# Performance work log

Measured on AMD Instinct MI355X. Metric: run time of the kernel, lower is better.

The kernel has to match this reference:

```python
import jax, jax.numpy as jnp
import numpy as np

N = 100000        # num_nodes
F_IN = 512        # node_features
F_OUT = 2         # GCNConv out channels (hardcoded in module)
E = 3200000       # num edges (avg degree 32)


def setup_inputs() -> dict:
    key = jax.random.key(0)
    k = jax.random.split(key, 8)
    x = jax.random.normal(k[0], (N, F_IN), dtype=jnp.float32)
    edge_list = jax.random.randint(k[1], (2, E), 0, N, dtype=jnp.int64)
    edge_attr = jax.random.uniform(k[2], (E,), dtype=jnp.float32)
    # GCNConv params (glorot-ish scale)
    W = jax.random.normal(k[3], (F_IN, F_OUT), dtype=jnp.float32) / np.sqrt(F_IN)
    b = jnp.zeros((F_OUT,), dtype=jnp.float32)
    # fc head: Linear(num_nodes*2, 1)
    fc_w = jax.random.normal(k[4], (N * F_OUT,), dtype=jnp.float32) / np.sqrt(N * F_OUT)
    fc_b = jnp.zeros((), dtype=jnp.float32)
    return {"x": x, "edge_list": edge_list, "edge_attr": edge_attr,
            "W": W, "b": b, "fc_w": fc_w, "fc_b": fc_b}


def reference(x, edge_list, edge_attr, W, b, fc_w, fc_b):
    n = x.shape[0]
    row, col = edge_list[0], edge_list[1]
    # --- gcn_norm with add_self_loops=True (fill weight 1.0) ---
    loop = jnp.arange(n, dtype=edge_list.dtype)
    row_f = jnp.concatenate([row, loop])
    col_f = jnp.concatenate([col, loop])
    w_f = jnp.concatenate([edge_attr, jnp.ones((n,), dtype=edge_attr.dtype)])
    deg = jax.ops.segment_sum(w_f, col_f, num_segments=n)          # [N]
    deg_inv_sqrt = jnp.where(deg > 0, jax.lax.rsqrt(jnp.maximum(deg, 1e-30)), 0.0)
    norm = deg_inv_sqrt[row_f] * w_f * deg_inv_sqrt[col_f]          # [E+N]
    # --- linear transform then propagate (source row -> target col) ---
    h = x @ W                                                       # [N, 2]
    msg = h[row_f] * norm[:, None]                                  # [E+N, 2]
    out = jax.ops.segment_sum(msg, col_f, num_segments=n) + b      # [N, 2]
    # --- head: relu, (no dropout/noise: training=False), flatten, fc, sigmoid ---
    out = jax.nn.relu(out).reshape(-1)                              # [2N]
    logit = jnp.dot(out, fc_w) + fc_b
    return jax.nn.sigmoid(logit)
```

## Files before the change

### kernel.cpp

```cpp
#include <hip/hip_runtime.h>
#include <math.h>

#define N_NODES 100000
#define F_IN    512
#define E_EDGES 3200000

#define NR   16
#define RN   6250
#define REP  32
#define CHUNK (E_EDGES / REP)


__global__ __launch_bounds__(1024) void k_deg_tiled(const int* __restrict__ col,
                                                    const float* __restrict__ w,
                                                    float* __restrict__ rep_deg) {
    __shared__ float sdeg[RN];
    int r = blockIdx.x / REP, p = blockIdx.x % REP;
    int r0 = r * RN;
    for (int j = threadIdx.x; j < RN; j += 1024) sdeg[j] = 0.0f;
    __syncthreads();
    const int*   colc = col + p * CHUNK;
    const float* wc   = w   + p * CHUNK;
    for (int e4 = threadIdx.x * 4; e4 < CHUNK; e4 += 4096) {
        int4 c4 = *(const int4*)(colc + e4);
#pragma unroll
        for (int q = 0; q < 4; ++q) {
            unsigned j = (unsigned)((&c4.x)[q] - r0);
            if (j < RN) atomicAdd(&sdeg[j], wc[e4 + q]);
        }
    }
    __syncthreads();
    float* out = rep_deg + (size_t)blockIdx.x * RN;
    for (int j = threadIdx.x; j < RN; j += 1024) out[j] = sdeg[j];
}

__global__ void k_dis(const float* __restrict__ rep_deg,
                      float* __restrict__ dis, float* __restrict__ logit) {
    int i = blockIdx.x * blockDim.x + threadIdx.x;
    if (i < N_NODES) {
        int r = i / RN, j = i - r * RN;
        const float* base = rep_deg + (size_t)(r * REP) * RN + j;
        float d = 1.0f;
#pragma unroll
        for (int p = 0; p < REP; ++p) d += base[p * RN];
        dis[i] = rsqrtf(d);
    }
    if (i == 0) logit[0] = 0.0f;
}

__global__ __launch_bounds__(256) void k_gemv(const float* __restrict__ x,
                                              const float* __restrict__ W,
                                              const float* __restrict__ dis,
                                              float* __restrict__ g) {
    int row  = (blockIdx.x * blockDim.x + threadIdx.x) >> 6;
    int lane = threadIdx.x & 63;
    if (row >= N_NODES) return;
    const float* xr = x + (size_t)row * F_IN;
    float a0 = 0.0f, a1 = 0.0f;
#pragma unroll
    for (int c = 0; c < 2; ++c) {
        int k = c * 256 + lane * 4;
        float4 xv  = *(const float4*)(xr + k);
        float4 w01 = *(const float4*)(W + 2 * k);
        float4 w23 = *(const float4*)(W + 2 * k + 4);
        a0 += xv.x * w01.x + xv.y * w01.z + xv.z * w23.x + xv.w * w23.z;
        a1 += xv.x * w01.y + xv.y * w01.w + xv.z * w23.y + xv.w * w23.w;
    }
#pragma unroll
    for (int off = 32; off > 0; off >>= 1) {
        a0 += __shfl_down(a0, off, 64);
        a1 += __shfl_down(a1, off, 64);
    }
    if (lane == 0) {
        float d = dis[row];
        g[2 * row] = a0 * d;
        g[2 * row + 1] = a1 * d;
    }
}

__global__ __launch_bounds__(1024) void k_prop_tiled(const int* __restrict__ row,
                                                     const int* __restrict__ col,
                                                     const float* __restrict__ w,
                                                     const float* __restrict__ g,
                                                     float* __restrict__ rep_acc) {
    __shared__ float sacc[RN * 2];
    int r = blockIdx.x / REP, p = blockIdx.x % REP;
    int r0 = r * RN;
    for (int j = threadIdx.x; j < RN * 2; j += 1024) sacc[j] = 0.0f;
    __syncthreads();
    const int*   colc = col + p * CHUNK;
    const int*   rowc = row + p * CHUNK;
    const float* wc   = w   + p * CHUNK;
    for (int e4 = threadIdx.x * 4; e4 < CHUNK; e4 += 4096) {
        int4 c4 = *(const int4*)(colc + e4);
#pragma unroll
        for (int q = 0; q < 4; ++q) {
            unsigned j = (unsigned)((&c4.x)[q] - r0);
            if (j < RN) {
                int e  = e4 + q;
                int rr = rowc[e];
                float we = wc[e];
                float2 gv = *(const float2*)(g + 2 * rr);
                atomicAdd(&sacc[2 * j],     gv.x * we);
                atomicAdd(&sacc[2 * j + 1], gv.y * we);
            }
        }
    }
    __syncthreads();
    float* out = rep_acc + (size_t)blockIdx.x * (RN * 2);
    for (int j = threadIdx.x; j < RN * 2; j += 1024) out[j] = sacc[j];
}

__global__ __launch_bounds__(256) void k_epilogue_tiled(const float* __restrict__ rep_acc,
                                                        const float* __restrict__ g,
                                                        const float* __restrict__ dis,
                                                        const float* __restrict__ b,
                                                        const float* __restrict__ fc_w,
                                                        float* __restrict__ logit) {
    int i = blockIdx.x * blockDim.x + threadIdx.x;
    float partial = 0.0f;
    if (i < N_NODES) {
        int r = i / RN, j = i - r * RN;
        const float2* base = (const float2*)rep_acc + (size_t)(r * REP) * RN + j;
        float o0 = 0.0f, o1 = 0.0f;
#pragma unroll
        for (int p = 0; p < REP; ++p) { float2 v = base[p * RN]; o0 += v.x; o1 += v.y; }
        float d = dis[i];
        o0 = (o0 + g[2 * i])     * d + b[0];
        o1 = (o1 + g[2 * i + 1]) * d + b[1];
        o0 = fmaxf(o0, 0.0f); o1 = fmaxf(o1, 0.0f);
        partial = o0 * fc_w[2 * i] + o1 * fc_w[2 * i + 1];
    }
#pragma unroll
    for (int off = 32; off > 0; off >>= 1)
        partial += __shfl_down(partial, off, 64);
    __shared__ float sdata[4];
    int lane = threadIdx.x & 63, wid = threadIdx.x >> 6;
    if (lane == 0) sdata[wid] = partial;
    __syncthreads();
    if (threadIdx.x == 0)
        atomicAdd(logit, sdata[0] + sdata[1] + sdata[2] + sdata[3]);
}

__global__ void k_sigmoid(const float* __restrict__ logit,
                          const float* __restrict__ fc_b,
                          float* __restrict__ out) {
    float z = logit[0] + fc_b[0];
    out[0] = 1.0f / (1.0f + expf(-z));
}


__global__ void k_init(float* __restrict__ deg, float* __restrict__ accum,
                       float* __restrict__ logit) {
    int i = blockIdx.x * blockDim.x + threadIdx.x;
    if (i < N_NODES) {
        deg[i] = 1.0f;
        accum[2 * i] = 0.0f;
        accum[2 * i + 1] = 0.0f;
    }
    if (i == 0) logit[0] = 0.0f;
}

__global__ void k_deg(const int* __restrict__ col, const float* __restrict__ w,
                      float* __restrict__ deg) {
    int e = blockIdx.x * blockDim.x + threadIdx.x;
    if (e < E_EDGES) atomicAdd(&deg[col[e]], w[e]);
}

__global__ void k_rsqrt(float* __restrict__ deg) {
    int i = blockIdx.x * blockDim.x + threadIdx.x;
    if (i < N_NODES) deg[i] = rsqrtf(deg[i]);
}

__global__ void k_gemv_h(const float* __restrict__ x, const float* __restrict__ W,
                         float* __restrict__ h) {
    int row  = (blockIdx.x * blockDim.x + threadIdx.x) >> 6;
    int lane = threadIdx.x & 63;
    if (row >= N_NODES) return;
    const float* xr = x + (size_t)row * F_IN;
    float a0 = 0.0f, a1 = 0.0f;
#pragma unroll
    for (int c = 0; c < 2; ++c) {
        int k = c * 256 + lane * 4;
        float4 xv  = *(const float4*)(xr + k);
        float4 w01 = *(const float4*)(W + 2 * k);
        float4 w23 = *(const float4*)(W + 2 * k + 4);
        a0 += xv.x * w01.x + xv.y * w01.z + xv.z * w23.x + xv.w * w23.z;
        a1 += xv.x * w01.y + xv.y * w01.w + xv.z * w23.y + xv.w * w23.w;
    }
#pragma unroll
    for (int off = 32; off > 0; off >>= 1) {
        a0 += __shfl_down(a0, off, 64);
        a1 += __shfl_down(a1, off, 64);
    }
    if (lane == 0) { h[2 * row] = a0; h[2 * row + 1] = a1; }
}

__global__ void k_prop(const int* __restrict__ row, const int* __restrict__ col,
                       const float* __restrict__ w, const float* __restrict__ dis,
                       const float* __restrict__ h, float* __restrict__ accum) {
    int e = blockIdx.x * blockDim.x + threadIdx.x;
    if (e < E_EDGES) {
        int r = row[e], c = col[e];
        float nm = dis[r] * w[e] * dis[c];
        atomicAdd(&accum[2 * c],     h[2 * r] * nm);
        atomicAdd(&accum[2 * c + 1], h[2 * r + 1] * nm);
    }
}

__global__ __launch_bounds__(256) void k_epilogue(const float* __restrict__ accum,
                                                  const float* __restrict__ h,
                                                  const float* __restrict__ dis,
                                                  const float* __restrict__ b,
                                                  const float* __restrict__ fc_w,
                                                  float* __restrict__ logit) {
    int i = blockIdx.x * blockDim.x + threadIdx.x;
    float partial = 0.0f;
    if (i < N_NODES) {
        float d2 = dis[i] * dis[i];
        float o0 = accum[2 * i]     + h[2 * i]     * d2 + b[0];
        float o1 = accum[2 * i + 1] + h[2 * i + 1] * d2 + b[1];
        o0 = fmaxf(o0, 0.0f); o1 = fmaxf(o1, 0.0f);
        partial = o0 * fc_w[2 * i] + o1 * fc_w[2 * i + 1];
    }
#pragma unroll
    for (int off = 32; off > 0; off >>= 1)
        partial += __shfl_down(partial, off, 64);
    __shared__ float sdata[4];
    int lane = threadIdx.x & 63, wid = threadIdx.x >> 6;
    if (lane == 0) sdata[wid] = partial;
    __syncthreads();
    if (threadIdx.x == 0)
        atomicAdd(logit, sdata[0] + sdata[1] + sdata[2] + sdata[3]);
}


extern "C" void kernel_launch(void* const* d_in, const int* in_sizes, int n_in,
                              void* d_out, int out_size, void* d_ws, size_t ws_size,
                              hipStream_t stream) {
    const float* x   = (const float*)d_in[0];
    const int*   el  = (const int*)d_in[1];
    const float* ea  = (const float*)d_in[2];
    const float* W   = (const float*)d_in[3];
    const float* b   = (const float*)d_in[4];
    const float* fcw = (const float*)d_in[5];
    const float* fcb = (const float*)d_in[6];
    float*       out = (float*)d_out;

    const int* row = el;
    const int* col = el + E_EDGES;

    float* ws = (float*)d_ws;
    const int TB = 256;
    dim3 gN((N_NODES + TB - 1) / TB);
    dim3 gG((N_NODES * 64 + TB - 1) / TB);

    const size_t need_fast = (size_t)(3 * N_NODES +
                                      (size_t)NR * REP * RN * 3 + 64) * 4;

    if (ws_size >= need_fast) {
        float* g       = ws;
        float* dis     = ws + 2 * N_NODES;
        float* rep_deg = ws + 3 * N_NODES;
        float* rep_acc = rep_deg + (size_t)NR * REP * RN;
        float* logit   = rep_acc + (size_t)NR * REP * RN * 2;

        k_deg_tiled     <<<NR * REP, 1024, 0, stream>>>(col, ea, rep_deg);
        k_dis           <<<gN, TB, 0, stream>>>(rep_deg, dis, logit);
        k_gemv          <<<gG, TB, 0, stream>>>(x, W, dis, g);
        k_prop_tiled    <<<NR * REP, 1024, 0, stream>>>(row, col, ea, g, rep_acc);
        k_epilogue_tiled<<<gN, TB, 0, stream>>>(rep_acc, g, dis, b, fcw, logit);
        k_sigmoid       <<<1, 1, 0, stream>>>(logit, fcb, out);
    } else {
        float* deg   = ws;
        float* h     = ws + N_NODES;
        float* accum = ws + 3 * N_NODES;
        float* logit = ws + 5 * N_NODES;
        dim3 gE((E_EDGES + TB - 1) / TB);
        k_init    <<<gN, TB, 0, stream>>>(deg, accum, logit);
        k_deg     <<<gE, TB, 0, stream>>>(col, ea, deg);
        k_rsqrt   <<<gN, TB, 0, stream>>>(deg);
        k_gemv_h  <<<gG, TB, 0, stream>>>(x, W, h);
        k_prop    <<<gE, TB, 0, stream>>>(row, col, ea, deg, h, accum);
        k_epilogue<<<gN, TB, 0, stream>>>(accum, h, deg, b, fcw, logit);
        k_sigmoid <<<1, 1, 0, stream>>>(logit, fcb, out);
    }
}
```

Measured before the change: 427.3 us.

## Bucket edges by destination range before degree and propagation passes

Adds a histogram, prefix-sum and scatter pass that groups edges by destination node range, packing the local target index and source row into one word. Degree and propagation blocks then each process only their own range's edges split into slices, instead of every block scanning a whole chunk and discarding most edges. This removes redundant edge reads at the cost of three extra kernels and an extra edge-sized write and read.

```diff
diff --git a/kernel.cpp b/kernel.cpp
--- a/kernel.cpp
+++ b/kernel.cpp
@@ -5,29 +5,88 @@
 #define F_IN    512
 #define E_EDGES 3200000
 
-#define NR   16
-#define RN   6250
-#define REP  32
-#define CHUNK (E_EDGES / REP)
-
-
-__global__ __launch_bounds__(1024) void k_deg_tiled(const int* __restrict__ col,
-                                                    const float* __restrict__ w,
-                                                    float* __restrict__ rep_deg) {
+#define NR     16
+#define RN     6250
+#define SB     512
+#define SCHUNK (E_EDGES / SB)
+#define SLICES 32
+#define JMASK  0x1FFF
+
+__global__ __launch_bounds__(256) void k_hist(const int* __restrict__ col,
+                                              int* __restrict__ cnt) {
+    __shared__ int hcnt[NR];
+    int t = threadIdx.x;
+    if (t < NR) hcnt[t] = 0;
+    __syncthreads();
+    int base = blockIdx.x * SCHUNK;
+    for (int i = t; i < SCHUNK; i += 256) {
+        int r = col[base + i] / RN;
+        atomicAdd(&hcnt[r], 1);
+    }
+    __syncthreads();
+    if (t < NR) cnt[t * SB + blockIdx.x] = hcnt[t];
+}
+
+__global__ __launch_bounds__(1024) void k_prefix(const int* __restrict__ cnt,
+                                                 int* __restrict__ off) {
+    __shared__ int psum[1024];
+    int t = threadIdx.x;
+    int v[8]; int s = 0;
+    int base = t * 8;
+#pragma unroll
+    for (int k = 0; k < 8; ++k) { v[k] = s; s += cnt[base + k]; }
+    psum[t] = s;
+    __syncthreads();
+    for (int d = 1; d < 1024; d <<= 1) {
+        int add = (t >= d) ? psum[t - d] : 0;
+        __syncthreads();
+        psum[t] += add;
+        __syncthreads();
+    }
+    int excl = psum[t] - s;
+#pragma unroll
+    for (int k = 0; k < 8; ++k) off[base + k] = excl + v[k];
+    if (t == 1023) off[NR * SB] = psum[1023];
+}
+
+__global__ __launch_bounds__(256) void k_scatter(const int* __restrict__ row,
+                                                 const int* __restrict__ col,
+                                                 const float* __restrict__ w,
+                                                 const int* __restrict__ off,
+                                                 unsigned* __restrict__ sidx,
+                                                 float* __restrict__ sw) {
+    __shared__ int cur[NR];
+    int t = threadIdx.x;
+    if (t < NR) cur[t] = off[t * SB + blockIdx.x];
+    __syncthreads();
+    int base = blockIdx.x * SCHUNK;
+    for (int i = t; i < SCHUNK; i += 256) {
+        int c  = col[base + i];
+        int rr = row[base + i];
+        float wv = w[base + i];
+        int r = c / RN;
+        int j = c - r * RN;
+        int slot = atomicAdd(&cur[r], 1);
+        sidx[slot] = (unsigned)j | ((unsigned)rr << 13);
+        sw[slot]   = wv;
+    }
+}
+
+__global__ __launch_bounds__(1024) void k_deg_s(const unsigned* __restrict__ sidx,
+                                                const float* __restrict__ sw,
+                                                const int* __restrict__ off,
+                                                float* __restrict__ rep_deg) {
     __shared__ float sdeg[RN];
-    int r = blockIdx.x / REP, p = blockIdx.x % REP;
-    int r0 = r * RN;
+    int r = blockIdx.x / SLICES, s = blockIdx.x % SLICES;
+    int lo_r = off[r * SB], hi_r = off[(r + 1) * SB];
+    int len = hi_r - lo_r;
+    int lo = lo_r + len * s / SLICES;
+    int hi = lo_r + len * (s + 1) / SLICES;
     for (int j = threadIdx.x; j < RN; j += 1024) sdeg[j] = 0.0f;
     __syncthreads();
-    const int*   colc = col + p * CHUNK;
-    const float* wc   = w   + p * CHUNK;
-    for (int e4 = threadIdx.x * 4; e4 < CHUNK; e4 += 4096) {
-        int4 c4 = *(const int4*)(colc + e4);
-#pragma unroll
-        for (int q = 0; q < 4; ++q) {
-            unsigned j = (unsigned)((&c4.x)[q] - r0);
-            if (j < RN) atomicAdd(&sdeg[j], wc[e4 + q]);
-        }
+    for (int i = lo + threadIdx.x; i < hi; i += 1024) {
+        unsigned u = sidx[i];
+        atomicAdd(&sdeg[u & JMASK], sw[i]);
     }
     __syncthreads();
     float* out = rep_deg + (size_t)blockIdx.x * RN;
@@ -39,10 +98,10 @@
     int i = blockIdx.x * blockDim.x + threadIdx.x;
     if (i < N_NODES) {
         int r = i / RN, j = i - r * RN;
-        const float* base = rep_deg + (size_t)(r * REP) * RN + j;
+        const float* base = rep_deg + (size_t)(r * SLICES) * RN + j;
         float d = 1.0f;
 #pragma unroll
-        for (int p = 0; p < REP; ++p) d += base[p * RN];
+        for (int p = 0; p < SLICES; ++p) d += base[p * RN];
         dis[i] = rsqrtf(d);
     }
     if (i == 0) logit[0] = 0.0f;
@@ -73,58 +132,52 @@
     }
     if (lane == 0) {
         float d = dis[row];
-        g[2 * row] = a0 * d;
+        g[2 * row]     = a0 * d;
         g[2 * row + 1] = a1 * d;
     }
 }
 
-__global__ __launch_bounds__(1024) void k_prop_tiled(const int* __restrict__ row,
-                                                     const int* __restrict__ col,
-                                                     const float* __restrict__ w,
-                                                     const float* __restrict__ g,
-                                                     float* __restrict__ rep_acc) {
+__global__ __launch_bounds__(1024) void k_prop_s(const unsigned* __restrict__ sidx,
+                                                 const float* __restrict__ sw,
+                                                 const int* __restrict__ off,
+                                                 const float* __restrict__ g,
+                                                 float* __restrict__ rep_acc) {
     __shared__ float sacc[RN * 2];
-    int r = blockIdx.x / REP, p = blockIdx.x % REP;
-    int r0 = r * RN;
+    int r = blockIdx.x / SLICES, s = blockIdx.x % SLICES;
+    int lo_r = off[r * SB], hi_r = off[(r + 1) * SB];
+    int len = hi_r - lo_r;
+    int lo = lo_r + len * s / SLICES;
+    int hi = lo_r + len * (s + 1) / SLICES;
     for (int j = threadIdx.x; j < RN * 2; j += 1024) sacc[j] = 0.0f;
     __syncthreads();
-    const int*   colc = col + p * CHUNK;
-    const int*   rowc = row + p * CHUNK;
-    const float* wc   = w   + p * CHUNK;
-    for (int e4 = threadIdx.x * 4; e4 < CHUNK; e4 += 4096) {
-        int4 c4 = *(const int4*)(colc + e4);
-#pragma unroll
-        for (int q = 0; q < 4; ++q) {
-            unsigned j = (unsigned)((&c4.x)[q] - r0);
-            if (j < RN) {
-                int e  = e4 + q;
-                int rr = rowc[e];
-                float we = wc[e];
-                float2 gv = *(const float2*)(g + 2 * rr);
-                atomicAdd(&sacc[2 * j],     gv.x * we);
-                atomicAdd(&sacc[2 * j + 1], gv.y * we);
-            }
-        }
+    for (int i = lo + threadIdx.x; i < hi; i += 1024) {
+        unsigned u = sidx[i];
+        int j  = u & JMASK;
+        int rr = u >> 13;
+        float we = sw[i];
+        float2 gv = *(const float2*)(g + 2 * rr);
+        atomicAdd(&sacc[2 * j],     gv.x * we);
+        atomicAdd(&sacc[2 * j + 1], gv.y * we);
     }
     __syncthreads();
     float* out = rep_acc + (size_t)blockIdx.x * (RN * 2);
     for (int j = threadIdx.x; j < RN * 2; j += 1024) out[j] = sacc[j];
 }
 
-__global__ __launch_bounds__(256) void k_epilogue_tiled(const float* __restrict__ rep_acc,
-                                                        const float* __restrict__ g,
-                                                        const float* __restrict__ dis,
-                                                        const float* __restrict__ b,
-                                                        const float* __restrict__ fc_w,
-                                                        float* __restrict__ logit) {
+__global__ __launch_bounds__(256) void k_epilogue(const float* __restrict__ rep_acc,
+                                                  const float* __restrict__ g,
+                                                  const float* __restrict__ dis,
+                                                  const float* __restrict__ b,
+                                                  const float* __restrict__ fc_w,
+                                                  float* __restrict__ logit) {
     int i = blockIdx.x * blockDim.x + threadIdx.x;
     float partial = 0.0f;
     if (i < N_NODES) {
         int r = i / RN, j = i - r * RN;
-        const float2* base = (const float2*)rep_acc + (size_t)(r * REP) * RN + j;
+        const float2* base = (const float2*)rep_acc + (size_t)(r * SLICES) * RN + j;
         float o0 = 0.0f, o1 = 0.0f;
 #pragma unroll
-        for (int p = 0; p < REP; ++p) { float2 v = base[p * RN]; o0 += v.x; o1 += v.y; }
+        for (int p = 0; p < SLICES; ++p) { float2 v = base[p * RN]; o0 += v.x; o1 += v.y; }
         float d = dis[i];
         o0 = (o0 + g[2 * i])     * d + b[0];
         o1 = (o1 + g[2 * i + 1]) * d + b[1];
@@ -150,8 +203,8 @@
 }
 
 
-__global__ void k_init(float* __restrict__ deg, float* __restrict__ accum,
-                       float* __restrict__ logit) {
+__global__ void k_init_f(float* __restrict__ deg, float* __restrict__ accum,
+                         float* __restrict__ logit) {
     int i = blockIdx.x * blockDim.x + threadIdx.x;
     if (i < N_NODES) {
         deg[i] = 1.0f;
@@ -161,65 +214,41 @@
     if (i == 0) logit[0] = 0.0f;
 }
 
-__global__ void k_deg(const int* __restrict__ col, const float* __restrict__ w,
-                      float* __restrict__ deg) {
+__global__ void k_deg_f(const int* __restrict__ col, const float* __restrict__ w,
+                        float* __restrict__ deg) {
     int e = blockIdx.x * blockDim.x + threadIdx.x;
     if (e < E_EDGES) atomicAdd(&deg[col[e]], w[e]);
 }
 
-__global__ void k_rsqrt(float* __restrict__ deg) {
+__global__ void k_rsqrt_f(float* __restrict__ deg) {
     int i = blockIdx.x * blockDim.x + threadIdx.x;
     if (i < N_NODES) deg[i] = rsqrtf(deg[i]);
 }
 
-__global__ void k_gemv_h(const float* __restrict__ x, const float* __restrict__ W,
-                         float* __restrict__ h) {
-    int row  = (blockIdx.x * blockDim.x + threadIdx.x) >> 6;
-    int lane = threadIdx.x & 63;
-    if (row >= N_NODES) return;
-    const float* xr = x + (size_t)row * F_IN;
-    float a0 = 0.0f, a1 = 0.0f;
-#pragma unroll
-    for (int c = 0; c < 2; ++c) {
-        int k = c * 256 + lane * 4;
-        float4 xv  = *(const float4*)(xr + k);
-        float4 w01 = *(const float4*)(W + 2 * k);
-        float4 w23 = *(const float4*)(W + 2 * k + 4);
-        a0 += xv.x * w01.x + xv.y * w01.z + xv.z * w23.x + xv.w * w23.z;
-        a1 += xv.x * w01.y + xv.y * w01.w + xv.z * w23.y + xv.w * w23.w;
-    }
-#pragma unroll
-    for (int off = 32; off > 0; off >>= 1) {
-        a0 += __shfl_down(a0, off, 64);
-        a1 += __shfl_down(a1, off, 64);
-    }
-    if (lane == 0) { h[2 * row] = a0; h[2 * row + 1] = a1; }
-}
-
-__global__ void k_prop(const int* __restrict__ row, const int* __restrict__ col,
-                       const float* __restrict__ w, const float* __restrict__ dis,
-                       const float* __restrict__ h, float* __restrict__ accum) {
+__global__ void k_prop_f(const int* __restrict__ row, const int* __restrict__ col,
+                         const float* __restrict__ w, const float* __restrict__ dis,
+                         const float* __restrict__ g, float* __restrict__ accum) {
     int e = blockIdx.x * blockDim.x + threadIdx.x;
     if (e < E_EDGES) {
         int r = row[e], c = col[e];
-        float nm = dis[r] * w[e] * dis[c];
-        atomicAdd(&accum[2 * c],     h[2 * r] * nm);
-        atomicAdd(&accum[2 * c + 1], h[2 * r + 1] * nm);
-    }
-}
-
-__global__ __launch_bounds__(256) void k_epilogue(const float* __restrict__ accum,
-                                                  const float* __restrict__ h,
-                                                  const float* __restrict__ dis,
-                                                  const float* __restrict__ b,
-                                                  const float* __restrict__ fc_w,
-                                                  float* __restrict__ logit) {
+        float nm = w[e];
+        atomicAdd(&accum[2 * c],     g[2 * r] * nm);
+        atomicAdd(&accum[2 * c + 1], g[2 * r + 1] * nm);
+    }
+}
+
+__global__ __launch_bounds__(256) void k_epilogue_f(const float* __restrict__ accum,
+                                                    const float* __restrict__ g,
+                                                    const float* __restrict__ dis,
+                                                    const float* __restrict__ b,
+                                                    const float* __restrict__ fc_w,
+                                                    float* __restrict__ logit) {
     int i = blockIdx.x * blockDim.x + threadIdx.x;
     float partial = 0.0f;
     if (i < N_NODES) {
-        float d2 = dis[i] * dis[i];
-        float o0 = accum[2 * i]     + h[2 * i]     * d2 + b[0];
-        float o1 = accum[2 * i + 1] + h[2 * i + 1] * d2 + b[1];
+        float d = dis[i];
+        float o0 = (accum[2 * i]     + g[2 * i])     * d + b[0];
+        float o1 = (accum[2 * i + 1] + g[2 * i + 1]) * d + b[1];
         o0 = fmaxf(o0, 0.0f); o1 = fmaxf(o1, 0.0f);
         partial = o0 * fc_w[2 * i] + o1 * fc_w[2 * i + 1];
     }
@@ -255,34 +284,49 @@
     dim3 gN((N_NODES + TB - 1) / TB);
     dim3 gG((N_NODES * 64 + TB - 1) / TB);
 
-    const size_t need_fast = (size_t)(3 * N_NODES +
-                                      (size_t)NR * REP * RN * 3 + 64) * 4;
+    size_t o_g    = 0;
+    size_t o_dis  = o_g + 2 * N_NODES;
+    size_t o_log  = o_dis + N_NODES;
+    size_t o_cnt  = (o_log + 64) & ~63ull;
+    size_t o_off  = o_cnt + NR * SB;
+    size_t o_sidx = (o_off + NR * SB + 1 + 63) & ~63ull;
+    size_t o_sw   = o_sidx + E_EDGES;
+    size_t o_rd   = o_sw + E_EDGES;
+    size_t o_ra   = o_rd + (size_t)NR * SLICES * RN;
+    size_t need_fast = (o_ra + (size_t)NR * SLICES * RN * 2) * 4;
 
     if (ws_size >= need_fast) {
-        float* g       = ws;
-        float* dis     = ws + 2 * N_NODES;
-        float* rep_deg = ws + 3 * N_NODES;
-        float* rep_acc = rep_deg + (size_t)NR * REP * RN;
-        float* logit   = rep_acc + (size_t)NR * REP * RN * 2;
-
-        k_deg_tiled     <<<NR * REP, 1024, 0, stream>>>(col, ea, rep_deg);
-        k_dis           <<<gN, TB, 0, stream>>>(rep_deg, dis, logit);
-        k_gemv          <<<gG, TB, 0, stream>>>(x, W, dis, g);
-        k_prop_tiled    <<<NR * REP, 1024, 0, stream>>>(row, col, ea, g, rep_acc);
-        k_epilogue_tiled<<<gN, TB, 0, stream>>>(rep_acc, g, dis, b, fcw, logit);
-        k_sigmoid       <<<1, 1, 0, stream>>>(logit, fcb, out);
+        float*    g       = ws + o_g;
+        float*    dis     = ws + o_dis;
+        float*    logit   = ws + o_log;
+        int*      cnt     = (int*)(ws + o_cnt);
+        int*      off     = (int*)(ws + o_off);
+        unsigned* sidx    = (unsigned*)(ws + o_sidx);
+        float*    sw      = ws + o_sw;
+        float*    rep_deg = ws + o_rd;
+        float*    rep_acc = ws + o_ra;
+
+        k_hist    <<<SB, 256, 0, stream>>>(col, cnt);
+        k_prefix  <<<1, 1024, 0, stream>>>(cnt, off);
+        k_scatter <<<SB, 256, 0, stream>>>(row, col, ea, off, sidx, sw);
+        k_deg_s   <<<NR * SLICES, 1024, 0, stream>>>(sidx, sw, off, rep_deg);
+        k_dis     <<<gN, TB, 0, stream>>>(rep_deg, dis, logit);
+        k_gemv    <<<gG, TB, 0, stream>>>(x, W, dis, g);
+        k_prop_s  <<<NR * SLICES, 1024, 0, stream>>>(sidx, sw, off, g, rep_acc);
+        k_epilogue<<<gN, TB, 0, stream>>>(rep_acc, g, dis, b, fcw, logit);
+        k_sigmoid <<<1, 1, 0, stream>>>(logit, fcb, out);
     } else {
         float* deg   = ws;
-        float* h     = ws + N_NODES;
+        float* g     = ws + N_NODES;
         float* accum = ws + 3 * N_NODES;
         float* logit = ws + 5 * N_NODES;
         dim3 gE((E_EDGES + TB - 1) / TB);
-        k_init    <<<gN, TB, 0, stream>>>(deg, accum, logit);
-        k_deg     <<<gE, TB, 0, stream>>>(col, ea, deg);
-        k_rsqrt   <<<gN, TB, 0, stream>>>(deg);
-        k_gemv_h  <<<gG, TB, 0, stream>>>(x, W, h);
-        k_prop    <<<gE, TB, 0, stream>>>(row, col, ea, deg, h, accum);
-        k_epilogue<<<gN, TB, 0, stream>>>(accum, h, deg, b, fcw, logit);
-        k_sigmoid <<<1, 1, 0, stream>>>(logit, fcb, out);
-    }
-}
+        k_init_f    <<<gN, TB, 0, stream>>>(deg, accum, logit);
+        k_deg_f     <<<gE, TB, 0, stream>>>(col, ea, deg);
+        k_rsqrt_f   <<<gN, TB, 0, stream>>>(deg);
+        k_gemv      <<<gG, TB, 0, stream>>>(x, W, deg, g);
+        k_prop_f    <<<gE, TB, 0, stream>>>(row, col, ea, deg, g, accum);
+        k_epilogue_f<<<gN, TB, 0, stream>>>(accum, g, deg, b, fcw, logit);
+        k_sigmoid   <<<1, 1, 0, stream>>>(logit, fcb, out);
+    }
+}
```

Result: faster. 411.2 us (-3.8%).
